# Performance work log

Hardware: AMD Instinct MI355X
Metric: run time of the kernel (lower is better)

## Reference

```python
import jax, jax.numpy as jnp
import numpy as np

PLANE_AXES = jnp.array([[[0., 1., 0.], [1., 0., 0.], [0., 0., 1.]],
                        [[0., 0., 1.], [1., 0., 0.], [0., 1., 0.]],
                        [[0., 1., 0.], [0., 0., 1.], [1., 0., 0.]]], dtype=jnp.float32)


def setup_inputs() -> dict:
    key = jax.random.key(0)
    k1, k2 = jax.random.split(key)
    M, C, R = 1048576, 32, 512
    coords = jax.random.uniform(k1, (M, 3), jnp.float32, -1.0, 1.0)
    triplane = jax.random.normal(k2, (1, 3, C, R, R), jnp.float32) * 0.1
    return {"coords": coords, "triplane": triplane}


def _bilinear_sample(plane, x, y):
    # plane: [C, R, R]; x, y: [M] pixel coords (align_corners=True mapping applied).
    # Matches torch grid_sample(mode='bilinear', padding_mode='zeros', align_corners=True).
    R = plane.shape[-1]
    x0 = jnp.floor(x)
    y0 = jnp.floor(y)
    x0i = x0.astype(jnp.int32)
    y0i = y0.astype(jnp.int32)
    wx1 = x - x0
    wx0 = 1.0 - wx1
    wy1 = y - y0
    wy0 = 1.0 - wy1

    def tap(xi, yi, w):
        valid = ((xi >= 0) & (xi < R) & (yi >= 0) & (yi < R)).astype(plane.dtype)
        xc = jnp.clip(xi, 0, R - 1)
        yc = jnp.clip(yi, 0, R - 1)
        return plane[:, yc, xc] * (w * valid)  # [C, M]

    return (tap(x0i, y0i, wx0 * wy0) + tap(x0i + 1, y0i, wx1 * wy0)
            + tap(x0i, y0i + 1, wx0 * wy1) + tap(x0i + 1, y0i + 1, wx1 * wy1))


def reference(coords, triplane):
    # coords: [M, 3]; triplane: [1, 3, C, R, R]
    _, P, C, R, _ = triplane.shape
    planes = jnp.clip(triplane.reshape(P, C, R, R), -1.0, 1.0)
    inv = jnp.linalg.inv(PLANE_AXES)  # [3, 3, 3]
    # project_onto_planes: bmm(coords, inv_planes), keep first two coords (x, y)
    proj = jnp.einsum('mc,pcd->pmd', coords, inv)[..., :2]  # [3, M, 2]
    px = (proj[..., 0] + 1.0) * 0.5 * (R - 1)  # align_corners=True
    py = (proj[..., 1] + 1.0) * 0.5 * (R - 1)
    feat = jax.vmap(_bilinear_sample)(planes, px, py)  # [3, C, M]
    return feat.sum(0).T  # [M, C] — sum across the 3 planes
```

## Files before the change

### kernel.cpp

```cpp
#include <hip/hip_runtime.h>
#include <hip/hip_bf16.h>
#include <stdint.h>

#define RES 512
#define CH  32
#define NP  3
#define NTEX (NP * RES * RES)
#define WS_BYTES ((size_t)NTEX * CH * sizeof(uint16_t))

static __device__ __forceinline__ uint16_t f2bf(float f) {
    union { float f; uint32_t u; } v; v.f = f;
    uint32_t u = v.u;
    uint32_t r = (u + 0x7fffu + ((u >> 16) & 1u)) >> 16;
    return (uint16_t)r;
}

__global__ __launch_bounds__(256) void k_transpose(const float* __restrict__ tri,
                                                   uint16_t* __restrict__ ws) {
    int t = blockIdx.x * 256 + threadIdx.x;
    if (t >= NTEX) return;
    int x = t & (RES - 1);
    int y = (t >> 9) & (RES - 1);
    int p = t >> 18;
    const float* src = tri + (size_t)p * CH * RES * RES + (size_t)y * RES + x;
    uint32_t packed[16];
#pragma unroll
    for (int i = 0; i < 16; ++i) {
        float f0 = src[(size_t)(2 * i + 0) * (RES * RES)];
        float f1 = src[(size_t)(2 * i + 1) * (RES * RES)];
        f0 = fminf(1.f, fmaxf(-1.f, f0));
        f1 = fminf(1.f, fmaxf(-1.f, f1));
        packed[i] = (uint32_t)f2bf(f0) | ((uint32_t)f2bf(f1) << 16);
    }
    uint4* dst = (uint4*)(ws + (size_t)t * CH);
#pragma unroll
    for (int i = 0; i < 4; ++i)
        dst[i] = make_uint4(packed[4 * i], packed[4 * i + 1], packed[4 * i + 2], packed[4 * i + 3]);
}

__global__ __launch_bounds__(256) void k_gather(const float* __restrict__ coords,
                                                const uint16_t* __restrict__ ws,
                                                float* __restrict__ out, int M) {
    int m = blockIdx.x * 256 + threadIdx.x;
    if (m >= M) return;
    float cx = coords[3 * m + 0];
    float cy = coords[3 * m + 1];
    float cz = coords[3 * m + 2];

    float acc[CH];
#pragma unroll
    for (int c = 0; c < CH; ++c) acc[c] = 0.f;

    float us[3] = {cy, cz, cy};
    float vs[3] = {cx, cx, cz};

#pragma unroll
    for (int p = 0; p < 3; ++p) {
        float px = (us[p] + 1.f) * (0.5f * (RES - 1));
        float py = (vs[p] + 1.f) * (0.5f * (RES - 1));
        float x0f = floorf(px), y0f = floorf(py);
        int x0 = (int)x0f, y0 = (int)y0f;
        float wx1 = px - x0f, wx0 = 1.f - wx1;
        float wy1 = py - y0f, wy0 = 1.f - wy1;
        int   xs[2]  = {x0, x0 + 1};
        int   ys[2]  = {y0, y0 + 1};
        float wxv[2] = {wx0, wx1};
        float wyv[2] = {wy0, wy1};
#pragma unroll
        for (int j = 0; j < 2; ++j) {
#pragma unroll
            for (int i = 0; i < 2; ++i) {
                int xi = xs[i], yi = ys[j];
                bool valid = (xi >= 0) & (xi < RES) & (yi >= 0) & (yi < RES);
                int xc = min(max(xi, 0), RES - 1);
                int yc = min(max(yi, 0), RES - 1);
                float w = valid ? (wxv[i] * wyv[j]) : 0.f;
                const uint4* tp = (const uint4*)(ws + (((size_t)p * RES + yc) * RES + xc) * CH);
#pragma unroll
                for (int q = 0; q < 4; ++q) {
                    uint4 d = tp[q];
                    uint32_t wwv[4] = {d.x, d.y, d.z, d.w};
#pragma unroll
                    for (int e = 0; e < 4; ++e) {
                        union { uint32_t u; float f; } lo, hi;
                        lo.u = wwv[e] << 16;
                        hi.u = wwv[e] & 0xffff0000u;
                        acc[q * 8 + 2 * e + 0] += w * lo.f;
                        acc[q * 8 + 2 * e + 1] += w * hi.f;
                    }
                }
            }
        }
    }

    float4* dst = (float4*)(out + (size_t)m * CH);
#pragma unroll
    for (int i = 0; i < 8; ++i)
        dst[i] = make_float4(acc[4 * i], acc[4 * i + 1], acc[4 * i + 2], acc[4 * i + 3]);
}

__global__ __launch_bounds__(256) void k_gather_direct(const float* __restrict__ coords,
                                                       const float* __restrict__ tri,
                                                       float* __restrict__ out, int M) {
    int m = blockIdx.x * 256 + threadIdx.x;
    if (m >= M) return;
    float cx = coords[3 * m + 0];
    float cy = coords[3 * m + 1];
    float cz = coords[3 * m + 2];
    float acc[CH];
#pragma unroll
    for (int c = 0; c < CH; ++c) acc[c] = 0.f;
    float us[3] = {cy, cz, cy};
    float vs[3] = {cx, cx, cz};
    for (int p = 0; p < 3; ++p) {
        float px = (us[p] + 1.f) * (0.5f * (RES - 1));
        float py = (vs[p] + 1.f) * (0.5f * (RES - 1));
        float x0f = floorf(px), y0f = floorf(py);
        int x0 = (int)x0f, y0 = (int)y0f;
        float wx1 = px - x0f, wx0 = 1.f - wx1;
        float wy1 = py - y0f, wy0 = 1.f - wy1;
        int   xs[2]  = {x0, x0 + 1};
        int   ys[2]  = {y0, y0 + 1};
        float wxv[2] = {wx0, wx1};
        float wyv[2] = {wy0, wy1};
        for (int j = 0; j < 2; ++j)
            for (int i = 0; i < 2; ++i) {
                int xi = xs[i], yi = ys[j];
                bool valid = (xi >= 0) & (xi < RES) & (yi >= 0) & (yi < RES);
                int xc = min(max(xi, 0), RES - 1);
                int yc = min(max(yi, 0), RES - 1);
                float w = valid ? (wxv[i] * wyv[j]) : 0.f;
                const float* base = tri + ((size_t)p * CH) * RES * RES + (size_t)yc * RES + xc;
#pragma unroll
                for (int c = 0; c < CH; ++c) {
                    float v = base[(size_t)c * RES * RES];
                    v = fminf(1.f, fmaxf(-1.f, v));
                    acc[c] += w * v;
                }
            }
    }
    float4* dst = (float4*)(out + (size_t)m * CH);
#pragma unroll
    for (int i = 0; i < 8; ++i)
        dst[i] = make_float4(acc[4 * i], acc[4 * i + 1], acc[4 * i + 2], acc[4 * i + 3]);
}

extern "C" void kernel_launch(void* const* d_in, const int* in_sizes, int n_in,
                              void* d_out, int out_size, void* d_ws, size_t ws_size,
                              hipStream_t stream) {
    const float* coords = (const float*)d_in[0];
    const float* tri    = (const float*)d_in[1];
    float* out          = (float*)d_out;
    int M = in_sizes[0] / 3;

    if (ws_size >= WS_BYTES) {
        uint16_t* ws = (uint16_t*)d_ws;
        k_transpose<<<(NTEX + 255) / 256, 256, 0, stream>>>(tri, ws);
        k_gather<<<(M + 255) / 256, 256, 0, stream>>>(coords, ws, out, M);
    } else {
        k_gather_direct<<<(M + 255) / 256, 256, 0, stream>>>(coords, tri, out, M);
    }
}
```

Measured before the change: 435.3 us.

## Split gather across four threads per point and vectorize transpose loads

Result: slower. 705.3 us (+62.0%).

```diff
diff --git a/kernel.cpp b/kernel.cpp
--- a/kernel.cpp
+++ b/kernel.cpp
@@ -8,6 +8,8 @@
 #define NTEX (NP * RES * RES)
 #define WS_BYTES ((size_t)NTEX * CH * sizeof(uint16_t))
 
+typedef float  nfloat4 __attribute__((ext_vector_type(4)));
+
 static __device__ __forceinline__ uint16_t f2bf(float f) {
     union { float f; uint32_t u; } v; v.f = f;
     uint32_t u = v.u;
@@ -17,39 +19,51 @@
 
 __global__ __launch_bounds__(256) void k_transpose(const float* __restrict__ tri,
                                                    uint16_t* __restrict__ ws) {
-    int t = blockIdx.x * 256 + threadIdx.x;
-    if (t >= NTEX) return;
-    int x = t & (RES - 1);
-    int y = (t >> 9) & (RES - 1);
-    int p = t >> 18;
-    const float* src = tri + (size_t)p * CH * RES * RES + (size_t)y * RES + x;
-    uint32_t packed[16];
+    int t4 = blockIdx.x * 256 + threadIdx.x;
+    if (t4 >= NTEX / 4) return;
+    int x4 = (t4 & (RES / 4 - 1)) * 4;
+    int y  = (t4 >> 7) & (RES - 1);
+    int p  = t4 >> 16;
+    const float* src = tri + (size_t)p * CH * RES * RES + (size_t)y * RES + x4;
+
+    uint32_t packed[4][16];
 #pragma unroll
-    for (int i = 0; i < 16; ++i) {
-        float f0 = src[(size_t)(2 * i + 0) * (RES * RES)];
-        float f1 = src[(size_t)(2 * i + 1) * (RES * RES)];
-        f0 = fminf(1.f, fmaxf(-1.f, f0));
-        f1 = fminf(1.f, fmaxf(-1.f, f1));
-        packed[i] = (uint32_t)f2bf(f0) | ((uint32_t)f2bf(f1) << 16);
+    for (int cp = 0; cp < 16; ++cp) {
+        float4 a = *(const float4*)(src + (size_t)(2 * cp + 0) * (RES * RES));
+        float4 b = *(const float4*)(src + (size_t)(2 * cp + 1) * (RES * RES));
+        float av[4] = {a.x, a.y, a.z, a.w};
+        float bv[4] = {b.x, b.y, b.z, b.w};
+#pragma unroll
+        for (int i = 0; i < 4; ++i) {
+            float f0 = fminf(1.f, fmaxf(-1.f, av[i]));
+            float f1 = fminf(1.f, fmaxf(-1.f, bv[i]));
+            packed[i][cp] = (uint32_t)f2bf(f0) | ((uint32_t)f2bf(f1) << 16);
+        }
     }
-    uint4* dst = (uint4*)(ws + (size_t)t * CH);
 #pragma unroll
-    for (int i = 0; i < 4; ++i)
-        dst[i] = make_uint4(packed[4 * i], packed[4 * i + 1], packed[4 * i + 2], packed[4 * i + 3]);
+    for (int i = 0; i < 4; ++i) {
+        uint4* dst = (uint4*)(ws + ((size_t)t4 * 4 + i) * CH);
+#pragma unroll
+        for (int q = 0; q < 4; ++q)
+            dst[q] = make_uint4(packed[i][4 * q], packed[i][4 * q + 1],
+                                packed[i][4 * q + 2], packed[i][4 * q + 3]);
+    }
 }
 
-__global__ __launch_bounds__(256) void k_gather(const float* __restrict__ coords,
-                                                const uint16_t* __restrict__ ws,
-                                                float* __restrict__ out, int M) {
-    int m = blockIdx.x * 256 + threadIdx.x;
+__global__ __launch_bounds__(256, 8) void k_gather(const float* __restrict__ coords,
+                                                   const uint16_t* __restrict__ ws,
+                                                   float* __restrict__ out, int M) {
+    int tid = blockIdx.x * 256 + threadIdx.x;
+    int m = tid >> 2;
+    int q = tid & 3;
     if (m >= M) return;
     float cx = coords[3 * m + 0];
     float cy = coords[3 * m + 1];
     float cz = coords[3 * m + 2];
 
-    float acc[CH];
+    float acc[8];
 #pragma unroll
-    for (int c = 0; c < CH; ++c) acc[c] = 0.f;
+    for (int c = 0; c < 8; ++c) acc[c] = 0.f;
 
     float us[3] = {cy, cz, cy};
     float vs[3] = {cx, cx, cz};
@@ -75,28 +89,26 @@
                 int xc = min(max(xi, 0), RES - 1);
                 int yc = min(max(yi, 0), RES - 1);
                 float w = valid ? (wxv[i] * wyv[j]) : 0.f;
-                const uint4* tp = (const uint4*)(ws + (((size_t)p * RES + yc) * RES + xc) * CH);
+                const uint4* tp = (const uint4*)(ws + (((size_t)p * RES + yc) * RES + xc) * CH + q * 8);
+                uint4 d = *tp;
+                uint32_t wwv[4] = {d.x, d.y, d.z, d.w};
 #pragma unroll
-                for (int q = 0; q < 4; ++q) {
-                    uint4 d = tp[q];
-                    uint32_t wwv[4] = {d.x, d.y, d.z, d.w};
-#pragma unroll
-                    for (int e = 0; e < 4; ++e) {
-                        union { uint32_t u; float f; } lo, hi;
-                        lo.u = wwv[e] << 16;
-                        hi.u = wwv[e] & 0xffff0000u;
-                        acc[q * 8 + 2 * e + 0] += w * lo.f;
-                        acc[q * 8 + 2 * e + 1] += w * hi.f;
-                    }
+                for (int e = 0; e < 4; ++e) {
+                    union { uint32_t u; float f; } lo, hi;
+                    lo.u = wwv[e] << 16;
+                    hi.u = wwv[e] & 0xffff0000u;
+                    acc[2 * e + 0] += w * lo.f;
+                    acc[2 * e + 1] += w * hi.f;
                 }
             }
         }
     }
 
-    float4* dst = (float4*)(out + (size_t)m * CH);
-#pragma unroll
-    for (int i = 0; i < 8; ++i)
-        dst[i] = make_float4(acc[4 * i], acc[4 * i + 1], acc[4 * i + 2], acc[4 * i + 3]);
+    nfloat4* dst = (nfloat4*)(out + (size_t)m * CH + q * 8);
+    nfloat4 v0 = {acc[0], acc[1], acc[2], acc[3]};
+    nfloat4 v1 = {acc[4], acc[5], acc[6], acc[7]};
+    __builtin_nontemporal_store(v0, dst);
+    __builtin_nontemporal_store(v1, dst + 1);
 }
 
 __global__ __launch_bounds__(256) void k_gather_direct(const float* __restrict__ coords,
@@ -155,8 +167,9 @@
 
     if (ws_size >= WS_BYTES) {
         uint16_t* ws = (uint16_t*)d_ws;
-        k_transpose<<<(NTEX + 255) / 256, 256, 0, stream>>>(tri, ws);
-        k_gather<<<(M + 255) / 256, 256, 0, stream>>>(coords, ws, out, M);
+        k_transpose<<<(NTEX / 4 + 255) / 256, 256, 0, stream>>>(tri, ws);
+        int nthreads = M * 4;
+        k_gather<<<(nthreads + 255) / 256, 256, 0, stream>>>(coords, ws, out, M);
     } else {
         k_gather_direct<<<(M + 255) / 256, 256, 0, stream>>>(coords, tri, out, M);
     }
```
